# Kernel optimization log

Hardware: AMD Instinct MI355X
Metric: run time of the kernel (lower is better)

Reference implementation:

```python
import jax, jax.numpy as jnp
import numpy as np
import math

EPS_NORM = 1e-12
BN_EPS = 1e-5


def _l2norm(x):
    n = jnp.sqrt(jnp.sum(x * x, axis=-1, keepdims=True))
    return x / jnp.maximum(n, EPS_NORM)


def setup_inputs() -> dict:
    key = jax.random.key(0)
    ks = jax.random.split(key, 16)
    b, c, t, l = 16, 32, 16, 256
    s = 0.05
    return {
        "x": jax.random.normal(ks[0], (b, c, t, l), jnp.float32),
        "q_w": jax.random.normal(ks[1], (c, c), jnp.float32) * s,
        "q_b": jax.random.normal(ks[2], (c,), jnp.float32) * s,
        "k_w": jax.random.normal(ks[3], (c, c), jnp.float32) * s,
        "k_b": jax.random.normal(ks[4], (c,), jnp.float32) * s,
        "v_w": jax.random.normal(ks[5], (c, c), jnp.float32) * s,
        "v_b": jax.random.normal(ks[6], (c,), jnp.float32) * s,
        "m_w": jax.random.normal(ks[7], (c, c), jnp.float32) * s,
        "m_b": jax.random.normal(ks[8], (c,), jnp.float32) * s,
        "pre_prompt": jax.random.normal(ks[9], (1, c, 1, l), jnp.float32) * s,
        "conv_w": jax.random.normal(ks[10], (c, c, 9, 1), jnp.float32) * s,
        "conv_b": jax.random.normal(ks[11], (c,), jnp.float32) * s,
        "bn_gamma": jnp.ones((c,), jnp.float32),
        "bn_beta": jnp.zeros((c,), jnp.float32),
        "lin_w": jax.random.normal(ks[12], (l, l), jnp.float32) * s,
        "lin_b": jax.random.normal(ks[13], (l,), jnp.float32) * s,
        "atten_flag": 1,
    }


def reference(x, q_w, q_b, k_w, k_b, v_w, v_b, m_w, m_b, pre_prompt,
              conv_w, conv_b, bn_gamma, bn_beta, lin_w, lin_b, atten_flag):
    b, c, t, l = x.shape
    nh = 8
    hd = c // nh

    xp = jnp.transpose(x, (0, 2, 3, 1))  # (b,t,l,c)

    def heads(w, bias):
        h = xp @ w.T + bias
        h = h.reshape(b, t, l, nh, hd).transpose(0, 1, 3, 2, 4)  # (b,t,nh,l,hd)
        return _l2norm(h)

    q = heads(q_w, q_b)
    k = heads(k_w, k_b)
    v = heads(v_w, v_b)

    atten = jnp.einsum('bthld,bthmd->bthlm', q, k) / math.sqrt(hd)
    atten = jax.nn.softmax(atten, axis=-1)
    o = jnp.einsum('bthlm,bthmd->bthld', atten, v)  # (b,t,nh,l,hd)
    o = o.transpose(0, 1, 3, 2, 4).reshape(b, t, l, c)
    o = o @ m_w.T + m_b
    xo = jnp.transpose(o, (0, 3, 1, 2))  # (b,c,t,l)

    pre = jnp.broadcast_to(pre_prompt, (b, c, 1, l))
    con = jnp.concatenate([xo[:, :, :8], pre], axis=2)  # (b,c,9,l)

    # ConvNormAct: Conv2d (VALID, kernel (9,1)) + BatchNorm2d (batch stats) + ReLU
    h = jax.lax.conv_general_dilated(
        con, conv_w, window_strides=(1, 1), padding='VALID',
        dimension_numbers=('NCHW', 'OIHW', 'NCHW'))  # (b,c,1,l)
    h = h + conv_b[None, :, None, None]
    mean = jnp.mean(h, axis=(0, 2, 3), keepdims=True)
    var = jnp.var(h, axis=(0, 2, 3), keepdims=True)
    h = (h - mean) * jax.lax.rsqrt(var + BN_EPS)
    h = h * bn_gamma[None, :, None, None] + bn_beta[None, :, None, None]
    h = jax.nn.relu(h)

    p = h @ lin_w.T + lin_b  # Linear over token_len axis
    p = xo[:, :, 2:3] - p
    return jnp.concatenate([xo[:, :, :8], p], axis=2)  # (b,c,9,l)
```

## Files before the change

### kernel.cpp

```cpp
#include <hip/hip_runtime.h>
#include <hip/hip_bf16.h>


typedef __fp16 h2 __attribute__((ext_vector_type(2)));

#define O_OFF  0u
#define XO_OFF 2097152u
#define H_OFF  6291456u
#define S_OFF  6815744u

__device__ __forceinline__ int probe_f32(const unsigned short* graw) {
    return graw[0] == 0;
}
template<typename T> __device__ __forceinline__ float ldv(const T* p, long i);
template<> __device__ __forceinline__ float ldv<float>(const float* p, long i) {
    return p[i];
}
template<> __device__ __forceinline__ float ldv<__hip_bfloat16>(const __hip_bfloat16* p, long i) {
    return __bfloat162float(p[i]);
}
template<typename T> __device__ __forceinline__ void stv(T* p, size_t i, float v);
template<> __device__ __forceinline__ void stv<float>(float* p, size_t i, float v) {
    p[i] = v;
}
template<> __device__ __forceinline__ void stv<__hip_bfloat16>(__hip_bfloat16* p, size_t i, float v) {
    p[i] = __float2bfloat16(v);
}
__device__ __forceinline__ h2 pkh2(float a, float b) {
    return __builtin_amdgcn_cvt_pkrtz(a, b);
}
__device__ __forceinline__ float bflo(unsigned int u) {
    union { unsigned int i; float f; } c; c.i = u << 16; return c.f;
}
__device__ __forceinline__ float bfhi(unsigned int u) {
    union { unsigned int i; float f; } c; c.i = u & 0xffff0000u; return c.f;
}
union KVrow { uint4 u; h2 h[4]; };

template<typename T>
__device__ __forceinline__ void attn_body(
    const T* __restrict__ x,
    const T* __restrict__ qw, const T* __restrict__ qb,
    const T* __restrict__ kw, const T* __restrict__ kb,
    const T* __restrict__ vw, const T* __restrict__ vb,
    unsigned short* __restrict__ O, uint4* KV,
    float (*WL)[4][32], float (*BL)[4])
{
    const int tid = threadIdx.x;
    const int blk = blockIdx.x;
    const int h  = blk & 7;
    const int bt = blk >> 3;
    const int b  = bt >> 3, t = bt & 7;
    const int h4 = h * 4;

    for (int e = tid; e < 384; e += 128) {
        int p = e >> 7, r = e & 127;
        const T* W = (p == 0) ? qw : ((p == 1) ? kw : vw);
        WL[p][r >> 5][r & 31] = ldv(W, (long)(h4 + (r >> 5)) * 32 + (r & 31));
    }
    if (tid < 12) {
        int p = tid >> 2, j = tid & 3;
        const T* B = (p == 0) ? qb : ((p == 1) ? kb : vb);
        BL[p][j] = ldv(B, h4 + j);
    }

    float xv0[32], xv1[32];
    #pragma unroll
    for (int c = 0; c < 32; c++) {
        const long xb = (((long)b * 32 + c) * 16 + t) * 256 + tid;
        xv0[c] = ldv(x, xb);
        xv1[c] = ldv(x, xb + 128);
    }
    __syncthreads();

    float4 pr0[3], pr1[3];
    #pragma unroll
    for (int p = 0; p < 3; p++) {
        float a0[4], a1[4];
        #pragma unroll
        for (int j = 0; j < 4; j++) { a0[j] = BL[p][j]; a1[j] = a0[j]; }
        #pragma unroll
        for (int c0 = 0; c0 < 32; c0 += 4) {
            float4 w0 = *(const float4*)&WL[p][0][c0];
            float4 w1 = *(const float4*)&WL[p][1][c0];
            float4 w2 = *(const float4*)&WL[p][2][c0];
            float4 w3 = *(const float4*)&WL[p][3][c0];
            const float* wj[4] = {(const float*)&w0, (const float*)&w1,
                                  (const float*)&w2, (const float*)&w3};
            #pragma unroll
            for (int cc = 0; cc < 4; cc++) {
                float x0 = xv0[c0+cc], x1 = xv1[c0+cc];
                #pragma unroll
                for (int j = 0; j < 4; j++) {
                    a0[j] = fmaf(x0, wj[j][cc], a0[j]);
                    a1[j] = fmaf(x1, wj[j][cc], a1[j]);
                }
            }
        }
        float s20 = a0[0]*a0[0] + a0[1]*a0[1] + a0[2]*a0[2] + a0[3]*a0[3];
        float s21 = a1[0]*a1[0] + a1[1]*a1[1] + a1[2]*a1[2] + a1[3]*a1[3];
        float i0 = 1.0f / fmaxf(sqrtf(s20), 1e-12f);
        float i1 = 1.0f / fmaxf(sqrtf(s21), 1e-12f);
        if (p == 0) { i0 *= 0.7213475204444817f; i1 *= 0.7213475204444817f; }
        pr0[p] = make_float4(a0[0]*i0, a0[1]*i0, a0[2]*i0, a0[3]*i0);
        pr1[p] = make_float4(a1[0]*i1, a1[1]*i1, a1[2]*i1, a1[3]*i1);
    }

    KVrow r0, r1;
    r0.h[0] = pkh2(pr0[1].x, pr0[1].y); r0.h[1] = pkh2(pr0[1].z, pr0[1].w);
    r0.h[2] = pkh2(pr0[2].x, pr0[2].y); r0.h[3] = pkh2(pr0[2].z, pr0[2].w);
    r1.h[0] = pkh2(pr1[1].x, pr1[1].y); r1.h[1] = pkh2(pr1[1].z, pr1[1].w);
    r1.h[2] = pkh2(pr1[2].x, pr1[2].y); r1.h[3] = pkh2(pr1[2].z, pr1[2].w);
    KV[tid]       = r0.u;
    KV[tid + 128] = r1.u;
    const float4 qa = pr0[0], qb4 = pr1[0];
    __syncthreads();

    float o0x=0.f,o0y=0.f,o0z=0.f,o0w=0.f,den0=0.f;
    float o1x=0.f,o1y=0.f,o1z=0.f,o1w=0.f,den1=0.f;
    #pragma unroll 8
    for (int m = 0; m < 256; m++) {
        KVrow kv; kv.u = KV[m];
        float k0 = (float)kv.h[0][0], k1 = (float)kv.h[0][1];
        float k2 = (float)kv.h[1][0], k3 = (float)kv.h[1][1];
        float sa = fmaf(qa.x, k0, fmaf(qa.y, k1, fmaf(qa.z, k2, qa.w * k3)));
        float sb = fmaf(qb4.x, k0, fmaf(qb4.y, k1, fmaf(qb4.z, k2, qb4.w * k3)));
        float ea = __builtin_amdgcn_exp2f(sa);
        float eb = __builtin_amdgcn_exp2f(sb);
        float vx = (float)kv.h[2][0], vy = (float)kv.h[2][1];
        float vz = (float)kv.h[3][0], vw = (float)kv.h[3][1];
        den0 += ea; den1 += eb;
        o0x = fmaf(ea, vx, o0x); o0y = fmaf(ea, vy, o0y);
        o0z = fmaf(ea, vz, o0z); o0w = fmaf(ea, vw, o0w);
        o1x = fmaf(eb, vx, o1x); o1y = fmaf(eb, vy, o1y);
        o1z = fmaf(eb, vz, o1z); o1w = fmaf(eb, vw, o1w);
    }
    float i0 = 1.0f / den0, i1 = 1.0f / den1;

    uint2 pk0, pk1;
    h2 a01 = pkh2(o0x*i0, o0y*i0), a23 = pkh2(o0z*i0, o0w*i0);
    h2 b01 = pkh2(o1x*i1, o1y*i1), b23 = pkh2(o1z*i1, o1w*i1);
    pk0.x = *(unsigned int*)&a01; pk0.y = *(unsigned int*)&a23;
    pk1.x = *(unsigned int*)&b01; pk1.y = *(unsigned int*)&b23;
    *(uint2*)(O + ((size_t)bt * 256u + tid) * 32u + h4)       = pk0;
    *(uint2*)(O + ((size_t)bt * 256u + tid + 128) * 32u + h4) = pk1;
}

__global__ __launch_bounds__(128) void k_attn(
    const void* __restrict__ x,
    const void* __restrict__ qw, const void* __restrict__ qb,
    const void* __restrict__ kw, const void* __restrict__ kb,
    const void* __restrict__ vw, const void* __restrict__ vb,
    unsigned short* __restrict__ O, float* __restrict__ sbuf,
    const unsigned short* __restrict__ graw)
{
    __shared__ uint4 KV[256];
    __shared__ float WL[3][4][32];
    __shared__ float BL[3][4];
    if (blockIdx.x == 0 && threadIdx.x < 64) sbuf[threadIdx.x] = 0.0f;
    if (probe_f32(graw))
        attn_body<float>((const float*)x, (const float*)qw, (const float*)qb,
                         (const float*)kw, (const float*)kb,
                         (const float*)vw, (const float*)vb, O, KV, WL, BL);
    else
        attn_body<__hip_bfloat16>((const __hip_bfloat16*)x,
                                  (const __hip_bfloat16*)qw, (const __hip_bfloat16*)qb,
                                  (const __hip_bfloat16*)kw, (const __hip_bfloat16*)kb,
                                  (const __hip_bfloat16*)vw, (const __hip_bfloat16*)vb,
                                  O, KV, WL, BL);
}

template<typename T>
__device__ __forceinline__ void mproj_body(
    const unsigned short* __restrict__ O,
    const T* __restrict__ mw, const T* __restrict__ mb,
    T* __restrict__ out, float* __restrict__ xof, float* sw, float* sb)
{
    const int tid = threadIdx.x;
    const int blk = blockIdx.x;
    const int bt = blk >> 1, lhalf = blk & 1;
    const int b = bt >> 3, t = bt & 7;
    const int l = lhalf * 128 + tid;

    for (int e = tid; e < 1024; e += 128) sw[e] = ldv(mw, e);
    if (tid < 32) sb[tid] = ldv(mb, tid);

    float ov[32];
    const unsigned short* src = O + ((size_t)bt * 256u + l) * 32u;
    #pragma unroll
    for (int cc = 0; cc < 4; cc++) {
        union { uint4 u; h2 h[4]; } uu;
        uu.u = *(const uint4*)(src + cc * 8);
        #pragma unroll
        for (int j = 0; j < 4; j++) {
            ov[cc*8 + 2*j]     = (float)uu.h[j][0];
            ov[cc*8 + 2*j + 1] = (float)uu.h[j][1];
        }
    }
    __syncthreads();

    #pragma unroll 4
    for (int co = 0; co < 32; co++) {
        float s = sb[co];
        #pragma unroll
        for (int c0 = 0; c0 < 32; c0 += 4) {
            float4 w4 = *(const float4*)&sw[co * 32 + c0];
            s = fmaf(ov[c0+0], w4.x, s);
            s = fmaf(ov[c0+1], w4.y, s);
            s = fmaf(ov[c0+2], w4.z, s);
            s = fmaf(ov[c0+3], w4.w, s);
        }
        stv(out, (((size_t)b * 32 + co) * 9 + t) * 256u + l, s);
        xof[(((size_t)b * 32 + co) * 8 + t) * 256u + l] = s;
    }
}

__global__ __launch_bounds__(128) void k_mproj(
    const unsigned short* __restrict__ O,
    const void* __restrict__ mw, const void* __restrict__ mb,
    void* __restrict__ out, float* __restrict__ xof,
    const unsigned short* __restrict__ graw)
{
    __shared__ float sw[1024];
    __shared__ float sb[32];
    if (probe_f32(graw))
        mproj_body<float>(O, (const float*)mw, (const float*)mb,
                          (float*)out, xof, sw, sb);
    else
        mproj_body<__hip_bfloat16>(O, (const __hip_bfloat16*)mw,
                                   (const __hip_bfloat16*)mb,
                                   (__hip_bfloat16*)out, xof, sw, sb);
}

template<typename T>
__device__ __forceinline__ void conv_body(
    const float* __restrict__ xof, const T* __restrict__ pre,
    const T* __restrict__ cw, const T* __restrict__ cb,
    float* __restrict__ hout, float* __restrict__ s, float* wl)
{
    const int tid = threadIdx.x;
    const int blk = blockIdx.x;
    const int b = blk >> 4, cog = (blk >> 1) & 7, lhalf = blk & 1;
    const int co0 = cog * 4;
    const int l = lhalf * 128 + tid;

    for (int e = tid; e < 1152; e += 128) {
        int g = e & 3, r = e >> 2;
        wl[e] = ldv(cw, (long)(co0 + g) * 288 + r);
    }
    __syncthreads();

    float a0 = 0.f, a1 = 0.f, a2 = 0.f, a3 = 0.f;
    #pragma unroll 4
    for (int ci = 0; ci < 32; ci++) {
        const float* xp = xof + (((size_t)b * 32 + ci) * 8) * 256u + l;
        float v[9];
        #pragma unroll
        for (int kt = 0; kt < 8; kt++) v[kt] = xp[kt * 256];
        v[8] = ldv(pre, (long)ci * 256 + l);
        #pragma unroll
        for (int kt = 0; kt < 9; kt++) {
            float4 w4 = *(const float4*)&wl[(ci * 9 + kt) * 4];
            a0 = fmaf(v[kt], w4.x, a0);
            a1 = fmaf(v[kt], w4.y, a1);
            a2 = fmaf(v[kt], w4.z, a2);
            a3 = fmaf(v[kt], w4.w, a3);
        }
    }
    a0 += ldv(cb, co0+0); a1 += ldv(cb, co0+1);
    a2 += ldv(cb, co0+2); a3 += ldv(cb, co0+3);

    hout[((size_t)b * 32 + co0 + 0) * 256u + l] = a0;
    hout[((size_t)b * 32 + co0 + 1) * 256u + l] = a1;
    hout[((size_t)b * 32 + co0 + 2) * 256u + l] = a2;
    hout[((size_t)b * 32 + co0 + 3) * 256u + l] = a3;

    float acc[4] = {a0, a1, a2, a3};
    #pragma unroll
    for (int g = 0; g < 4; g++) {
        float sg = acc[g], sq = acc[g] * acc[g];
        #pragma unroll
        for (int off = 32; off > 0; off >>= 1) {
            sg += __shfl_down(sg, off, 64);
            sq += __shfl_down(sq, off, 64);
        }
        if ((tid & 63) == 0) {
            atomicAdd(&s[co0 + g], sg);
            atomicAdd(&s[32 + co0 + g], sq);
        }
    }
}

__global__ __launch_bounds__(128) void k_conv(
    const float* __restrict__ xof, const void* __restrict__ pre,
    const void* __restrict__ cw, const void* __restrict__ cb,
    float* __restrict__ hout, float* __restrict__ s,
    const unsigned short* __restrict__ graw)
{
    __shared__ float wl[1152];
    if (probe_f32(graw))
        conv_body<float>(xof, (const float*)pre, (const float*)cw,
                         (const float*)cb, hout, s, wl);
    else
        conv_body<__hip_bfloat16>(xof, (const __hip_bfloat16*)pre,
                                  (const __hip_bfloat16*)cw,
                                  (const __hip_bfloat16*)cb, hout, s, wl);
}

__device__ __forceinline__ float rowdot(const float* rp, const float* hn) {
    float acc = 0.f;
    #pragma unroll 4
    for (int i0 = 0; i0 < 256; i0 += 4) {
        float4 u = *(const float4*)(rp + i0);
        acc = fmaf(hn[i0+0], u.x, acc);
        acc = fmaf(hn[i0+1], u.y, acc);
        acc = fmaf(hn[i0+2], u.z, acc);
        acc = fmaf(hn[i0+3], u.w, acc);
    }
    return acc;
}
__device__ __forceinline__ float rowdot(const __hip_bfloat16* rp_, const float* hn) {
    const unsigned short* rp = (const unsigned short*)rp_;
    float acc = 0.f;
    #pragma unroll 2
    for (int i0 = 0; i0 < 256; i0 += 16) {
        uint4 u0 = *(const uint4*)(rp + i0);
        uint4 u1 = *(const uint4*)(rp + i0 + 8);
        unsigned int uu[8] = {u0.x, u0.y, u0.z, u0.w, u1.x, u1.y, u1.z, u1.w};
        #pragma unroll
        for (int j = 0; j < 8; j++) {
            acc = fmaf(hn[i0 + 2*j],     bflo(uu[j]), acc);
            acc = fmaf(hn[i0 + 2*j + 1], bfhi(uu[j]), acc);
        }
    }
    return acc;
}

template<typename T>
__device__ __forceinline__ void lin_body(
    const float* __restrict__ hbuf, const float* __restrict__ s,
    const T* __restrict__ gam, const T* __restrict__ bet,
    const T* __restrict__ lw, const T* __restrict__ lb,
    const float* __restrict__ xof, T* __restrict__ out, float* hn)
{
    const int tid = threadIdx.x;
    const int blk = blockIdx.x;
    const int b = blk >> 5, co = blk & 31;

    float mean = s[co] * (1.0f / 4096.0f);
    float var  = fmaxf(s[32 + co] * (1.0f / 4096.0f) - mean * mean, 0.0f);
    float sc = ldv(gam, co) * __frsqrt_rn(var + 1e-5f);
    float sh = ldv(bet, co) - mean * sc;

    float hv = hbuf[(size_t)blk * 256u + tid];
    hn[tid] = fmaxf(fmaf(hv, sc, sh), 0.0f);
    __syncthreads();

    float acc = rowdot(lw + (size_t)tid * 256u, hn) + ldv(lb, tid);

    float xo2 = xof[(((size_t)b * 32 + co) * 8 + 2) * 256u + tid];
    stv(out, (((size_t)b * 32 + co) * 9 + 8) * 256u + tid, xo2 - acc);
}

__global__ __launch_bounds__(256) void k_lin(
    const float* __restrict__ hbuf, const float* __restrict__ s,
    const void* __restrict__ gam, const void* __restrict__ bet,
    const void* __restrict__ lw, const void* __restrict__ lb,
    const float* __restrict__ xof, void* __restrict__ out,
    const unsigned short* __restrict__ graw)
{
    __shared__ float hn[256];
    if (probe_f32(graw))
        lin_body<float>(hbuf, s, (const float*)gam, (const float*)bet,
                        (const float*)lw, (const float*)lb, xof, (float*)out, hn);
    else
        lin_body<__hip_bfloat16>(hbuf, s, (const __hip_bfloat16*)gam,
                                 (const __hip_bfloat16*)bet,
                                 (const __hip_bfloat16*)lw,
                                 (const __hip_bfloat16*)lb, xof,
                                 (__hip_bfloat16*)out, hn);
}

extern "C" void kernel_launch(void* const* d_in, const int* in_sizes, int n_in,
                              void* d_out, int out_size, void* d_ws, size_t ws_size,
                              hipStream_t stream) {
    const unsigned short* graw = (const unsigned short*)d_in[12];

    unsigned short* Obuf = (unsigned short*)((char*)d_ws + O_OFF);
    float* xof  = (float*)((char*)d_ws + XO_OFF);
    float* hbuf = (float*)((char*)d_ws + H_OFF);
    float* sbuf = (float*)((char*)d_ws + S_OFF);

    k_attn <<<1024, 128, 0, stream>>>(d_in[0], d_in[1], d_in[2], d_in[3],
                                      d_in[4], d_in[5], d_in[6],
                                      Obuf, sbuf, graw);
    k_mproj<<<256,  128, 0, stream>>>(Obuf, d_in[7], d_in[8], d_out, xof, graw);
    k_conv <<<256,  128, 0, stream>>>(xof, d_in[9], d_in[10], d_in[11],
                                      hbuf, sbuf, graw);
    k_lin  <<<512,  256, 0, stream>>>(hbuf, sbuf, d_in[12], d_in[13],
                                      d_in[14], d_in[15], xof, d_out, graw);
}
```

Before: 190.1 us.

## Fuse four kernels into one cooperative kernel with grid syncs; packed fp16 attention math

Merges the attention, output-projection, conv+BN-stats and linear kernels into a single cooperative launch separated by grid.sync barriers. The goal is to remove per-kernel launch gaps and tail drain between stages, with a fallback to separate launches if the cooperative launch fails. The attention inner loop now uses fdot2 for Q·K and packed half-precision accumulation for the P·V sum, which cuts instruction count but accumulates in fp16 and so loses precision. The linear stage is reshaped to 128 threads handling two outputs each, so it matches the fused block size.

```diff
diff --git a/kernel.cpp b/kernel.cpp
--- a/kernel.cpp
+++ b/kernel.cpp
@@ -1,5 +1,8 @@
 #include <hip/hip_runtime.h>
 #include <hip/hip_bf16.h>
+#include <hip/hip_cooperative_groups.h>
+
+namespace cg = cooperative_groups;
 
 
 typedef __fp16 h2 __attribute__((ext_vector_type(2)));
@@ -35,22 +38,33 @@
 __device__ __forceinline__ float bfhi(unsigned int u) {
     union { unsigned int i; float f; } c; c.i = u & 0xffff0000u; return c.f;
 }
+#if __has_builtin(__builtin_amdgcn_fdot2)
+__device__ __forceinline__ float fdot2(h2 a, h2 b, float c) {
+    return __builtin_amdgcn_fdot2(a, b, c, false);
+}
+#else
+__device__ __forceinline__ float fdot2(h2 a, h2 b, float c) {
+    return fmaf((float)a[0], (float)b[0], fmaf((float)a[1], (float)b[1], c));
+}
+#endif
 union KVrow { uint4 u; h2 h[4]; };
 
 template<typename T>
-__device__ __forceinline__ void attn_body(
+__device__ __forceinline__ void attn_phase(
     const T* __restrict__ x,
     const T* __restrict__ qw, const T* __restrict__ qb,
     const T* __restrict__ kw, const T* __restrict__ kb,
     const T* __restrict__ vw, const T* __restrict__ vb,
-    unsigned short* __restrict__ O, uint4* KV,
-    float (*WL)[4][32], float (*BL)[4])
-{
+    unsigned short* __restrict__ O, char* smem)
+{
+    uint4* KV = (uint4*)smem;
+    float (*WL)[4][32] = (float (*)[4][32])(smem + 4096);
+    float (*BL)[4]     = (float (*)[4])(smem + 5632);
+
     const int tid = threadIdx.x;
     const int blk = blockIdx.x;
-    const int h  = blk & 7;
-    const int bt = blk >> 3;
-    const int b  = bt >> 3, t = bt & 7;
+    const int h = blk & 7, bt = blk >> 3;
+    const int b = bt >> 3, t = bt & 7;
     const int h4 = h * 4;
 
     for (int e = tid; e < 384; e += 128) {
@@ -113,69 +127,41 @@
     r1.h[2] = pkh2(pr1[2].x, pr1[2].y); r1.h[3] = pkh2(pr1[2].z, pr1[2].w);
     KV[tid]       = r0.u;
     KV[tid + 128] = r1.u;
-    const float4 qa = pr0[0], qb4 = pr1[0];
+    const h2 qa01 = pkh2(pr0[0].x, pr0[0].y), qa23 = pkh2(pr0[0].z, pr0[0].w);
+    const h2 qb01 = pkh2(pr1[0].x, pr1[0].y), qb23 = pkh2(pr1[0].z, pr1[0].w);
     __syncthreads();
 
-    float o0x=0.f,o0y=0.f,o0z=0.f,o0w=0.f,den0=0.f;
-    float o1x=0.f,o1y=0.f,o1z=0.f,o1w=0.f,den1=0.f;
+    h2 o01a = pkh2(0.f, 0.f), o23a = o01a, o01b = o01a, o23b = o01a;
+    float den0 = 0.f, den1 = 0.f;
     #pragma unroll 8
     for (int m = 0; m < 256; m++) {
         KVrow kv; kv.u = KV[m];
-        float k0 = (float)kv.h[0][0], k1 = (float)kv.h[0][1];
-        float k2 = (float)kv.h[1][0], k3 = (float)kv.h[1][1];
-        float sa = fmaf(qa.x, k0, fmaf(qa.y, k1, fmaf(qa.z, k2, qa.w * k3)));
-        float sb = fmaf(qb4.x, k0, fmaf(qb4.y, k1, fmaf(qb4.z, k2, qb4.w * k3)));
+        float sa = fdot2(qa01, kv.h[0], fdot2(qa23, kv.h[1], 0.0f));
+        float sb = fdot2(qb01, kv.h[0], fdot2(qb23, kv.h[1], 0.0f));
         float ea = __builtin_amdgcn_exp2f(sa);
         float eb = __builtin_amdgcn_exp2f(sb);
-        float vx = (float)kv.h[2][0], vy = (float)kv.h[2][1];
-        float vz = (float)kv.h[3][0], vw = (float)kv.h[3][1];
         den0 += ea; den1 += eb;
-        o0x = fmaf(ea, vx, o0x); o0y = fmaf(ea, vy, o0y);
-        o0z = fmaf(ea, vz, o0z); o0w = fmaf(ea, vw, o0w);
-        o1x = fmaf(eb, vx, o1x); o1y = fmaf(eb, vy, o1y);
-        o1z = fmaf(eb, vz, o1z); o1w = fmaf(eb, vw, o1w);
+        h2 epa = pkh2(ea, ea), epb = pkh2(eb, eb);
+        o01a += epa * kv.h[2]; o23a += epa * kv.h[3];
+        o01b += epb * kv.h[2]; o23b += epb * kv.h[3];
     }
     float i0 = 1.0f / den0, i1 = 1.0f / den1;
-
-    uint2 pk0, pk1;
-    h2 a01 = pkh2(o0x*i0, o0y*i0), a23 = pkh2(o0z*i0, o0w*i0);
-    h2 b01 = pkh2(o1x*i1, o1y*i1), b23 = pkh2(o1z*i1, o1w*i1);
-    pk0.x = *(unsigned int*)&a01; pk0.y = *(unsigned int*)&a23;
-    pk1.x = *(unsigned int*)&b01; pk1.y = *(unsigned int*)&b23;
-    *(uint2*)(O + ((size_t)bt * 256u + tid) * 32u + h4)       = pk0;
-    *(uint2*)(O + ((size_t)bt * 256u + tid + 128) * 32u + h4) = pk1;
-}
-
-__global__ __launch_bounds__(128) void k_attn(
-    const void* __restrict__ x,
-    const void* __restrict__ qw, const void* __restrict__ qb,
-    const void* __restrict__ kw, const void* __restrict__ kb,
-    const void* __restrict__ vw, const void* __restrict__ vb,
-    unsigned short* __restrict__ O, float* __restrict__ sbuf,
-    const unsigned short* __restrict__ graw)
-{
-    __shared__ uint4 KV[256];
-    __shared__ float WL[3][4][32];
-    __shared__ float BL[3][4];
-    if (blockIdx.x == 0 && threadIdx.x < 64) sbuf[threadIdx.x] = 0.0f;
-    if (probe_f32(graw))
-        attn_body<float>((const float*)x, (const float*)qw, (const float*)qb,
-                         (const float*)kw, (const float*)kb,
-                         (const float*)vw, (const float*)vb, O, KV, WL, BL);
-    else
-        attn_body<__hip_bfloat16>((const __hip_bfloat16*)x,
-                                  (const __hip_bfloat16*)qw, (const __hip_bfloat16*)qb,
-                                  (const __hip_bfloat16*)kw, (const __hip_bfloat16*)kb,
-                                  (const __hip_bfloat16*)vw, (const __hip_bfloat16*)vb,
-                                  O, KV, WL, BL);
+    h2 ia = pkh2(i0, i0), ib = pkh2(i1, i1);
+    union { h2 h; unsigned int u; } c0, c1, c2, c3;
+    c0.h = o01a * ia; c1.h = o23a * ia;
+    c2.h = o01b * ib; c3.h = o23b * ib;
+    *(uint2*)(O + ((size_t)bt * 256u + tid) * 32u + h4)       = make_uint2(c0.u, c1.u);
+    *(uint2*)(O + ((size_t)bt * 256u + tid + 128) * 32u + h4) = make_uint2(c2.u, c3.u);
 }
 
 template<typename T>
-__device__ __forceinline__ void mproj_body(
+__device__ __forceinline__ void mproj_phase(
     const unsigned short* __restrict__ O,
     const T* __restrict__ mw, const T* __restrict__ mb,
-    T* __restrict__ out, float* __restrict__ xof, float* sw, float* sb)
-{
+    T* __restrict__ out, float* __restrict__ xof, char* smem)
+{
+    float* sw = (float*)smem;
+    float* sb = (float*)(smem + 4096);
     const int tid = threadIdx.x;
     const int blk = blockIdx.x;
     const int bt = blk >> 1, lhalf = blk & 1;
@@ -215,29 +201,13 @@
     }
 }
 
-__global__ __launch_bounds__(128) void k_mproj(
-    const unsigned short* __restrict__ O,
-    const void* __restrict__ mw, const void* __restrict__ mb,
-    void* __restrict__ out, float* __restrict__ xof,
-    const unsigned short* __restrict__ graw)
-{
-    __shared__ float sw[1024];
-    __shared__ float sb[32];
-    if (probe_f32(graw))
-        mproj_body<float>(O, (const float*)mw, (const float*)mb,
-                          (float*)out, xof, sw, sb);
-    else
-        mproj_body<__hip_bfloat16>(O, (const __hip_bfloat16*)mw,
-                                   (const __hip_bfloat16*)mb,
-                                   (__hip_bfloat16*)out, xof, sw, sb);
-}
-
 template<typename T>
-__device__ __forceinline__ void conv_body(
+__device__ __forceinline__ void conv_phase(
     const float* __restrict__ xof, const T* __restrict__ pre,
     const T* __restrict__ cw, const T* __restrict__ cb,
-    float* __restrict__ hout, float* __restrict__ s, float* wl)
-{
+    float* __restrict__ hout, float* __restrict__ s, char* smem)
+{
+    float* wl = (float*)smem;
     const int tid = threadIdx.x;
     const int blk = blockIdx.x;
     const int b = blk >> 4, cog = (blk >> 1) & 7, lhalf = blk & 1;
@@ -289,22 +259,6 @@
             atomicAdd(&s[32 + co0 + g], sq);
         }
     }
-}
-
-__global__ __launch_bounds__(128) void k_conv(
-    const float* __restrict__ xof, const void* __restrict__ pre,
-    const void* __restrict__ cw, const void* __restrict__ cb,
-    float* __restrict__ hout, float* __restrict__ s,
-    const unsigned short* __restrict__ graw)
-{
-    __shared__ float wl[1152];
-    if (probe_f32(graw))
-        conv_body<float>(xof, (const float*)pre, (const float*)cw,
-                         (const float*)cb, hout, s, wl);
-    else
-        conv_body<__hip_bfloat16>(xof, (const __hip_bfloat16*)pre,
-                                  (const __hip_bfloat16*)cw,
-                                  (const __hip_bfloat16*)cb, hout, s, wl);
 }
 
 __device__ __forceinline__ float rowdot(const float* rp, const float* hn) {
@@ -337,66 +291,184 @@
 }
 
 template<typename T>
-__device__ __forceinline__ void lin_body(
-    const float* __restrict__ hbuf, const float* __restrict__ s,
+__device__ __forceinline__ void lin_phase(
+    const float* __restrict__ hbuf, const float* __restrict__ sbuf,
     const T* __restrict__ gam, const T* __restrict__ bet,
     const T* __restrict__ lw, const T* __restrict__ lb,
-    const float* __restrict__ xof, T* __restrict__ out, float* hn)
-{
+    const float* __restrict__ xof, T* __restrict__ out, char* smem)
+{
+    float* hn = (float*)smem;
     const int tid = threadIdx.x;
     const int blk = blockIdx.x;
     const int b = blk >> 5, co = blk & 31;
 
-    float mean = s[co] * (1.0f / 4096.0f);
-    float var  = fmaxf(s[32 + co] * (1.0f / 4096.0f) - mean * mean, 0.0f);
+    float mean = sbuf[co] * (1.0f / 4096.0f);
+    float var  = fmaxf(sbuf[32 + co] * (1.0f / 4096.0f) - mean * mean, 0.0f);
     float sc = ldv(gam, co) * __frsqrt_rn(var + 1e-5f);
     float sh = ldv(bet, co) - mean * sc;
 
-    float hv = hbuf[(size_t)blk * 256u + tid];
-    hn[tid] = fmaxf(fmaf(hv, sc, sh), 0.0f);
+    const size_t hb = (size_t)blk * 256u;
+    hn[tid]       = fmaxf(fmaf(hbuf[hb + tid], sc, sh), 0.0f);
+    hn[tid + 128] = fmaxf(fmaf(hbuf[hb + tid + 128], sc, sh), 0.0f);
     __syncthreads();
 
-    float acc = rowdot(lw + (size_t)tid * 256u, hn) + ldv(lb, tid);
-
-    float xo2 = xof[(((size_t)b * 32 + co) * 8 + 2) * 256u + tid];
-    stv(out, (((size_t)b * 32 + co) * 9 + 8) * 256u + tid, xo2 - acc);
-}
-
-__global__ __launch_bounds__(256) void k_lin(
-    const float* __restrict__ hbuf, const float* __restrict__ s,
-    const void* __restrict__ gam, const void* __restrict__ bet,
-    const void* __restrict__ lw, const void* __restrict__ lb,
-    const float* __restrict__ xof, void* __restrict__ out,
-    const unsigned short* __restrict__ graw)
-{
-    __shared__ float hn[256];
+    float acc0 = rowdot(lw + (size_t)tid * 256u, hn) + ldv(lb, tid);
+    float acc1 = rowdot(lw + (size_t)(tid + 128) * 256u, hn) + ldv(lb, tid + 128);
+
+    const size_t xb = (((size_t)b * 32 + co) * 8 + 2) * 256u;
+    const size_t ob = (((size_t)b * 32 + co) * 9 + 8) * 256u;
+    stv(out, ob + tid,       xof[xb + tid] - acc0);
+    stv(out, ob + tid + 128, xof[xb + tid + 128] - acc1);
+}
+
+template<typename T>
+__device__ __forceinline__ void run_pipeline(
+    const T* x, const T* qw, const T* qb, const T* kw, const T* kb,
+    const T* vw, const T* vb, const T* mw, const T* mb, const T* pre,
+    const T* cw, const T* cb, const T* gam, const T* bet, const T* lw,
+    const T* lb, unsigned short* O, float* xof, float* hbuf, float* sbuf,
+    T* out, char* smem, cg::grid_group& grid)
+{
+    attn_phase<T>(x, qw, qb, kw, kb, vw, vb, O, smem);
+    if (blockIdx.x == 1023 && threadIdx.x < 64) sbuf[threadIdx.x] = 0.0f;
+    __threadfence();
+    grid.sync();
+    if (blockIdx.x < 256) mproj_phase<T>(O, mw, mb, out, xof, smem);
+    __threadfence();
+    grid.sync();
+    if (blockIdx.x < 256) conv_phase<T>(xof, pre, cw, cb, hbuf, sbuf, smem);
+    __threadfence();
+    grid.sync();
+    if (blockIdx.x < 512) lin_phase<T>(hbuf, sbuf, gam, bet, lw, lb, xof, out, smem);
+}
+
+__global__ __launch_bounds__(128, 2) void k_all(
+    const void* x, const void* qw, const void* qb, const void* kw,
+    const void* kb, const void* vw, const void* vb, const void* mw,
+    const void* mb, const void* pre, const void* cw, const void* cb,
+    const void* gam, const void* bet, const void* lw, const void* lb,
+    unsigned short* O, float* xof, float* hbuf, float* sbuf,
+    void* out, const unsigned short* graw)
+{
+    __shared__ __align__(16) char smem[6144];
+    cg::grid_group grid = cg::this_grid();
     if (probe_f32(graw))
-        lin_body<float>(hbuf, s, (const float*)gam, (const float*)bet,
-                        (const float*)lw, (const float*)lb, xof, (float*)out, hn);
+        run_pipeline<float>((const float*)x, (const float*)qw, (const float*)qb,
+            (const float*)kw, (const float*)kb, (const float*)vw, (const float*)vb,
+            (const float*)mw, (const float*)mb, (const float*)pre,
+            (const float*)cw, (const float*)cb, (const float*)gam,
+            (const float*)bet, (const float*)lw, (const float*)lb,
+            O, xof, hbuf, sbuf, (float*)out, smem, grid);
     else
-        lin_body<__hip_bfloat16>(hbuf, s, (const __hip_bfloat16*)gam,
-                                 (const __hip_bfloat16*)bet,
-                                 (const __hip_bfloat16*)lw,
-                                 (const __hip_bfloat16*)lb, xof,
-                                 (__hip_bfloat16*)out, hn);
+        run_pipeline<__hip_bfloat16>((const __hip_bfloat16*)x,
+            (const __hip_bfloat16*)qw, (const __hip_bfloat16*)qb,
+            (const __hip_bfloat16*)kw, (const __hip_bfloat16*)kb,
+            (const __hip_bfloat16*)vw, (const __hip_bfloat16*)vb,
+            (const __hip_bfloat16*)mw, (const __hip_bfloat16*)mb,
+            (const __hip_bfloat16*)pre, (const __hip_bfloat16*)cw,
+            (const __hip_bfloat16*)cb, (const __hip_bfloat16*)gam,
+            (const __hip_bfloat16*)bet, (const __hip_bfloat16*)lw,
+            (const __hip_bfloat16*)lb,
+            O, xof, hbuf, sbuf, (__hip_bfloat16*)out, smem, grid);
+}
+
+__global__ __launch_bounds__(128) void k_attn_s(
+    const void* x, const void* qw, const void* qb, const void* kw,
+    const void* kb, const void* vw, const void* vb,
+    unsigned short* O, float* sbuf, const unsigned short* graw)
+{
+    __shared__ __align__(16) char smem[6144];
+    if (blockIdx.x == 1023 && threadIdx.x < 64) sbuf[threadIdx.x] = 0.0f;
+    if (probe_f32(graw))
+        attn_phase<float>((const float*)x, (const float*)qw, (const float*)qb,
+            (const float*)kw, (const float*)kb, (const float*)vw,
+            (const float*)vb, O, smem);
+    else
+        attn_phase<__hip_bfloat16>((const __hip_bfloat16*)x,
+            (const __hip_bfloat16*)qw, (const __hip_bfloat16*)qb,
+            (const __hip_bfloat16*)kw, (const __hip_bfloat16*)kb,
+            (const __hip_bfloat16*)vw, (const __hip_bfloat16*)vb, O, smem);
+}
+__global__ __launch_bounds__(128) void k_mproj_s(
+    const unsigned short* O, const void* mw, const void* mb,
+    void* out, float* xof, const unsigned short* graw)
+{
+    __shared__ __align__(16) char smem[6144];
+    if (probe_f32(graw))
+        mproj_phase<float>(O, (const float*)mw, (const float*)mb,
+                           (float*)out, xof, smem);
+    else
+        mproj_phase<__hip_bfloat16>(O, (const __hip_bfloat16*)mw,
+                                    (const __hip_bfloat16*)mb,
+                                    (__hip_bfloat16*)out, xof, smem);
+}
+__global__ __launch_bounds__(128) void k_conv_s(
+    const float* xof, const void* pre, const void* cw, const void* cb,
+    float* hbuf, float* sbuf, const unsigned short* graw)
+{
+    __shared__ __align__(16) char smem[6144];
+    if (probe_f32(graw))
+        conv_phase<float>(xof, (const float*)pre, (const float*)cw,
+                          (const float*)cb, hbuf, sbuf, smem);
+    else
+        conv_phase<__hip_bfloat16>(xof, (const __hip_bfloat16*)pre,
+                                   (const __hip_bfloat16*)cw,
+                                   (const __hip_bfloat16*)cb, hbuf, sbuf, smem);
+}
+__global__ __launch_bounds__(128) void k_lin_s(
+    const float* hbuf, const float* sbuf, const void* gam, const void* bet,
+    const void* lw, const void* lb, const float* xof, void* out,
+    const unsigned short* graw)
+{
+    __shared__ __align__(16) char smem[6144];
+    if (probe_f32(graw))
+        lin_phase<float>(hbuf, sbuf, (const float*)gam, (const float*)bet,
+                         (const float*)lw, (const float*)lb, xof,
+                         (float*)out, smem);
+    else
+        lin_phase<__hip_bfloat16>(hbuf, sbuf, (const __hip_bfloat16*)gam,
+                                  (const __hip_bfloat16*)bet,
+                                  (const __hip_bfloat16*)lw,
+                                  (const __hip_bfloat16*)lb, xof,
+                                  (__hip_bfloat16*)out, smem);
 }
 
 extern "C" void kernel_launch(void* const* d_in, const int* in_sizes, int n_in,
                               void* d_out, int out_size, void* d_ws, size_t ws_size,
                               hipStream_t stream) {
+    const void* x   = d_in[0];
+    const void* qw  = d_in[1];  const void* qb  = d_in[2];
+    const void* kw  = d_in[3];  const void* kb  = d_in[4];
+    const void* vw  = d_in[5];  const void* vb  = d_in[6];
+    const void* mw  = d_in[7];  const void* mb  = d_in[8];
+    const void* pre = d_in[9];
+    const void* cw  = d_in[10]; const void* cb  = d_in[11];
+    const void* gam = d_in[12]; const void* bet = d_in[13];
+    const void* lw  = d_in[14]; const void* lb  = d_in[15];
     const unsigned short* graw = (const unsigned short*)d_in[12];
 
     unsigned short* Obuf = (unsigned short*)((char*)d_ws + O_OFF);
     float* xof  = (float*)((char*)d_ws + XO_OFF);
     float* hbuf = (float*)((char*)d_ws + H_OFF);
     float* sbuf = (float*)((char*)d_ws + S_OFF);
-
-    k_attn <<<1024, 128, 0, stream>>>(d_in[0], d_in[1], d_in[2], d_in[3],
-                                      d_in[4], d_in[5], d_in[6],
-                                      Obuf, sbuf, graw);
-    k_mproj<<<256,  128, 0, stream>>>(Obuf, d_in[7], d_in[8], d_out, xof, graw);
-    k_conv <<<256,  128, 0, stream>>>(xof, d_in[9], d_in[10], d_in[11],
-                                      hbuf, sbuf, graw);
-    k_lin  <<<512,  256, 0, stream>>>(hbuf, sbuf, d_in[12], d_in[13],
-                                      d_in[14], d_in[15], xof, d_out, graw);
-}
+    void* outp = d_out;
+
+    void* args[22] = {
+        (void*)&x,  (void*)&qw, (void*)&qb, (void*)&kw, (void*)&kb,
+        (void*)&vw, (void*)&vb, (void*)&mw, (void*)&mb, (void*)&pre,
+        (void*)&cw, (void*)&cb, (void*)&gam, (void*)&bet, (void*)&lw,
+        (void*)&lb, (void*)&Obuf, (void*)&xof, (void*)&hbuf, (void*)&sbuf,
+        (void*)&outp, (void*)&graw
+    };
+    hipError_t err = hipLaunchCooperativeKernel((void*)k_all, dim3(1024),
+                                                dim3(128), args, 0, stream);
+    if (err != hipSuccess) {
+        (void)hipGetLastError();
+        k_attn_s <<<1024, 128, 0, stream>>>(x, qw, qb, kw, kb, vw, vb,
+                                            Obuf, sbuf, graw);
+        k_mproj_s<<<256,  128, 0, stream>>>(Obuf, mw, mb, d_out, xof, graw);
+        k_conv_s <<<256,  128, 0, stream>>>(xof, pre, cw, cb, hbuf, sbuf, graw);
+        k_lin_s  <<<512,  128, 0, stream>>>(hbuf, sbuf, gam, bet, lw, lb,
+                                            xof, d_out, graw);
+    }
+}
```

New measurement: 664.7 us. 3.5x slower.
